# Performance work log

Hardware: AMD Instinct MI355X
Metric: run time of the kernel (lower is better)

Reference implementation:

```python
import jax, jax.numpy as jnp
import numpy as np
from jax import lax

NUM_GROUP = 512
GROUP_SIZE = 32


def setup_inputs() -> dict:
    key = jax.random.key(0)
    x = jax.random.normal(key, (8, 16384, 13), dtype=jnp.float32)
    return {"x": x}


def _fps(pts, num_group):
    """Farthest point sampling. pts: [B,N,3] -> centers [B,G,3], idx [B,G].
    Deterministic start at point 0 (as in pointnet2 CUDA fps)."""
    B, N, _ = pts.shape
    init_idx = jnp.zeros((B,), dtype=jnp.int32)

    def step(carry, _):
        min_d, last = carry                      # [B,N], [B]
        last_pt = jnp.take_along_axis(pts, last[:, None, None], axis=1)  # [B,1,3]
        d = jnp.sum((pts - last_pt) ** 2, axis=-1)                        # [B,N]
        min_d = jnp.minimum(min_d, d)
        nxt = jnp.argmax(min_d, axis=1).astype(jnp.int32)                 # [B]
        return (min_d, nxt), nxt

    init_d = jnp.full((B, N), 1e10, dtype=pts.dtype)
    _, rest = lax.scan(step, (init_d, init_idx), None, length=num_group - 1)  # [G-1,B]
    idx = jnp.concatenate([init_idx[None, :], rest], axis=0).T                # [B,G]
    centers = jnp.take_along_axis(pts, idx[:, :, None], axis=1)               # [B,G,3]
    return centers, idx


def _knn_idx(pts, centers, k):
    """k nearest points (in pts) to each center. pts [B,N,3], centers [B,G,3] -> [B,G,k]."""
    # squared distances [B,G,N] via ||c||^2 + ||p||^2 - 2 c.p
    d2 = (jnp.sum(centers ** 2, -1)[:, :, None]
          + jnp.sum(pts ** 2, -1)[:, None, :]
          - 2.0 * jnp.einsum('bgc,bnc->bgn', centers, pts))
    _, idx = lax.top_k(-d2, k)  # smallest distances
    return idx


def reference(x):
    B, N, C = x.shape
    pts = x[:, :, 4:7]                                  # [B,N,3]
    center_xyz, _ = _fps(pts, NUM_GROUP)                # [B,G,3]
    idx = _knn_idx(pts, center_xyz, GROUP_SIZE)         # [B,G,M]
    # gather neighborhoods: [B,G,M,C]
    flat_idx = idx.reshape(B, NUM_GROUP * GROUP_SIZE)
    neigh = jnp.take_along_axis(x, flat_idx[:, :, None], axis=1)
    neigh = neigh.reshape(B, NUM_GROUP, GROUP_SIZE, C)
    # recenter xyz channels 4:7
    neigh = neigh.at[:, :, :, 4:7].add(-center_xyz[:, :, None, :])
    return neigh, center_xyz
```

## Files before the change

### kernel.cpp

```cpp
#include <hip/hip_runtime.h>
#include <stdint.h>
#include <math.h>

#define BB 8
#define NN 16384
#define CC 13
#define GG 512
#define KK 32

#define NEIGH_ELEMS (BB*GG*KK*CC)

__device__ __forceinline__ void wave_argmax_dpp(float& v, int& p) {
    int vi = __float_as_int(v);
    int pi = p;
#define ARGMAX_STAGE(CTRL)                                                   \
    {                                                                        \
        int nv = __builtin_amdgcn_update_dpp(vi, vi, CTRL, 0xF, 0xF, false); \
        int np = __builtin_amdgcn_update_dpp(pi, pi, CTRL, 0xF, 0xF, false); \
        float a = __int_as_float(nv);                                        \
        float b = __int_as_float(vi);                                        \
        if (a > b || (a == b && np < pi)) { vi = nv; pi = np; }              \
    }
    ARGMAX_STAGE(0x111)
    ARGMAX_STAGE(0x112)
    ARGMAX_STAGE(0x114)
    ARGMAX_STAGE(0x118)
    ARGMAX_STAGE(0x142)
    ARGMAX_STAGE(0x143)
#undef ARGMAX_STAGE
    v = __int_as_float(vi);
    p = pi;
}

__device__ __forceinline__ void wave_argmin_dpp(float& v, int& p) {
    int vi = __float_as_int(v);
    int pi = p;
#define ARGMIN_STAGE(CTRL)                                                   \
    {                                                                        \
        int nv = __builtin_amdgcn_update_dpp(vi, vi, CTRL, 0xF, 0xF, false); \
        int np = __builtin_amdgcn_update_dpp(pi, pi, CTRL, 0xF, 0xF, false); \
        float a = __int_as_float(nv);                                        \
        float b = __int_as_float(vi);                                        \
        if (a < b || (a == b && np < pi)) { vi = nv; pi = np; }              \
    }
    ARGMIN_STAGE(0x111)
    ARGMIN_STAGE(0x112)
    ARGMIN_STAGE(0x114)
    ARGMIN_STAGE(0x118)
    ARGMIN_STAGE(0x142)
    ARGMIN_STAGE(0x143)
#undef ARGMIN_STAGE
    v = __int_as_float(vi);
    p = pi;
}

__global__ void pack_kernel(const float* __restrict__ x,
                            float* __restrict__ px, float* __restrict__ py,
                            float* __restrict__ pz) {
    int i = blockIdx.x * blockDim.x + threadIdx.x;
    if (i >= BB * NN) return;
    const float* p = x + (size_t)i * CC + 4;
    px[i] = p[0]; py[i] = p[1]; pz[i] = p[2];
}

__global__ __launch_bounds__(1024)
__attribute__((amdgpu_waves_per_eu(4, 4)))
void fps_kernel(const float* __restrict__ px,
                const float* __restrict__ py,
                const float* __restrict__ pz,
                float* __restrict__ centers) {
    const int b = blockIdx.x;
    const int t = threadIdx.x;
    const float* PX = px + b * NN;
    const float* PY = py + b * NN;
    const float* PZ = pz + b * NN;

#define DECLPT(i) float x##i, y##i, z##i, md##i;
    DECLPT(0)  DECLPT(1)  DECLPT(2)  DECLPT(3)
    DECLPT(4)  DECLPT(5)  DECLPT(6)  DECLPT(7)
    DECLPT(8)  DECLPT(9)  DECLPT(10) DECLPT(11)
    DECLPT(12) DECLPT(13) DECLPT(14) DECLPT(15)
#undef DECLPT

#define INITPT(i)                                                            \
    {                                                                        \
        int pos = t + (i << 10);                                             \
        x##i = PX[pos]; y##i = PY[pos]; z##i = PZ[pos];                      \
        md##i = 1e10f;                           \
        asm volatile("" : "+v"(x##i), "+v"(y##i), "+v"(z##i));               \
    }
    INITPT(0)  INITPT(1)  INITPT(2)  INITPT(3)
    INITPT(4)  INITPT(5)  INITPT(6)  INITPT(7)
    INITPT(8)  INITPT(9)  INITPT(10) INITPT(11)
    INITPT(12) INITPT(13) INITPT(14) INITPT(15)
#undef INITPT

    __shared__ float s_v[2][16];
    __shared__ int   s_p[2][16];

    int wp = 0;
    if (t == 0) {
        float* oc = centers + (size_t)b * GG * 3;
        oc[0] = PX[0]; oc[1] = PY[0]; oc[2] = PZ[0];
    }

    for (int g = 1; g < GG; ++g) {
        int swp = __builtin_amdgcn_readfirstlane(wp);
        float lx = PX[swp], ly = PY[swp], lz = PZ[swp];
        float bv = -1.0f;
        int bi = 0;
#define STEPPT(i)                                                            \
    {                                                                        \
        float e0 = __fsub_rn(x##i, lx);                                      \
        float e1 = __fsub_rn(y##i, ly);                                      \
        float e2 = __fsub_rn(z##i, lz);                                      \
        float d  = __fadd_rn(__fadd_rn(__fmul_rn(e0, e0), __fmul_rn(e1, e1)),\
                             __fmul_rn(e2, e2));                             \
        float m = fminf(md##i, d);                           \
        md##i = m;                                                           \
        if (m > bv) { bv = m; bi = i; }                                      \
    }
        STEPPT(0)  STEPPT(1)  STEPPT(2)  STEPPT(3)
        STEPPT(4)  STEPPT(5)  STEPPT(6)  STEPPT(7)
        STEPPT(8)  STEPPT(9)  STEPPT(10) STEPPT(11)
        STEPPT(12) STEPPT(13) STEPPT(14) STEPPT(15)
#undef STEPPT
        int bp = t + (bi << 10);
        wave_argmax_dpp(bv, bp);
        int par = g & 1;
        if ((t & 63) == 63) { s_v[par][t >> 6] = bv; s_p[par][t >> 6] = bp; }
        __syncthreads();
        float wv = s_v[par][0]; int wi = s_p[par][0];
#pragma unroll
        for (int q = 1; q < 16; ++q) {
            float qv = s_v[par][q]; int qp = s_p[par][q];
            if (qv > wv || (qv == wv && qp < wi)) { wv = qv; wi = qp; }
        }
        wp = wi;
        if (t == 0) {
            float* oc = centers + ((size_t)b * GG + g) * 3;
            oc[0] = PX[wp]; oc[1] = PY[wp]; oc[2] = PZ[wp];
        }
    }
}

__global__ __launch_bounds__(256, 8) void knn_kernel(const float* __restrict__ px,
                                                     const float* __restrict__ py,
                                                     const float* __restrict__ pz,
                                                     const float* __restrict__ x,
                                                     const float* __restrict__ centers,
                                                     float* __restrict__ out) {
    const int blk = blockIdx.x;
    const int bg  = ((blk & 7) << 9) | (blk >> 3);
    const int b   = bg >> 9;
    const int t   = threadIdx.x;

    const float* ctr = centers + (size_t)bg * 3;
    float cx = ctr[0], cy = ctr[1], cz = ctr[2];
    float cc2 = __fadd_rn(__fadd_rn(__fmul_rn(cx, cx), __fmul_rn(cy, cy)),
                          __fmul_rn(cz, cz));

    const float* PX = px + b * NN;
    const float* PY = py + b * NN;
    const float* PZ = pz + b * NN;

    float k1 = INFINITY, k2 = INFINITY;
    int   p1 = 0x7fffffff, p2 = 0x7fffffff;
    uint64_t mask = 0;

#pragma unroll 4
    for (int i = 0; i < 64; ++i) {
        int pos = (i << 8) + t;
        float ax = PX[pos], ay = PY[pos], az = PZ[pos];
        float pp2 = __fadd_rn(__fadd_rn(__fmul_rn(ax, ax), __fmul_rn(ay, ay)),
                              __fmul_rn(az, az));
        float dot = fmaf(cz, az, fmaf(cy, ay, __fmul_rn(cx, ax)));
        float d2  = __fsub_rn(__fadd_rn(cc2, pp2), __fmul_rn(2.0f, dot));
        if (d2 < k1)      { k2 = k1; p2 = p1; k1 = d2; p1 = pos; }
        else if (d2 < k2) { k2 = d2; p2 = pos; }
    }

    __shared__ float s_v[2][4];
    __shared__ int   s_p[2][4];
    __shared__ int   s_chosen[KK];

    for (int j = 0; j < KK; ++j) {
        float v = k1; int vp = p1;
        wave_argmin_dpp(v, vp);
        int par = j & 1;
        if ((t & 63) == 63) { s_v[par][t >> 6] = v; s_p[par][t >> 6] = vp; }
        __syncthreads();
        float wv = s_v[par][0]; int wp = s_p[par][0];
#pragma unroll
        for (int q = 1; q < 4; ++q) {
            float qv = s_v[par][q]; int qp = s_p[par][q];
            if (qv < wv || (qv == wv && qp < wp)) { wv = qv; wp = qp; }
        }
        if (t == 0) s_chosen[j] = wp;
        if ((wp & 255) == t) {
            mask |= 1ull << (wp >> 8);
            k1 = k2; p1 = p2;
            k2 = INFINITY; p2 = 0x7fffffff;
            if (p1 == 0x7fffffff && mask != 0xffffffffffffffffull) {
                k1 = INFINITY;
#pragma unroll 1
                for (int i = 0; i < 64; ++i) {
                    if ((mask >> i) & 1ull) continue;
                    int pos = (i << 8) + t;
                    float ax = PX[pos], ay = PY[pos], az = PZ[pos];
                    float pp2 = __fadd_rn(__fadd_rn(__fmul_rn(ax, ax), __fmul_rn(ay, ay)),
                                          __fmul_rn(az, az));
                    float dot = fmaf(cz, az, fmaf(cy, ay, __fmul_rn(cx, ax)));
                    float d2  = __fsub_rn(__fadd_rn(cc2, pp2), __fmul_rn(2.0f, dot));
                    if (d2 < k1)      { k2 = k1; p2 = p1; k1 = d2; p1 = pos; }
                    else if (d2 < k2) { k2 = d2; p2 = pos; }
                }
            }
        }
    }
    __syncthreads();

    for (int v = t; v < KK * CC; v += 256) {
        int j = v / CC, c = v - j * CC;
        int pt = s_chosen[j] & (NN - 1);
        float val = x[((size_t)b * NN + pt) * CC + c];
        if (c >= 4 && c < 7) {
            float cs = (c == 4) ? cx : ((c == 5) ? cy : cz);
            val = __fsub_rn(val, cs);
        }
        out[((size_t)bg * KK + j) * CC + c] = val;
    }
}

extern "C" void kernel_launch(void* const* d_in, const int* in_sizes, int n_in,
                              void* d_out, int out_size, void* d_ws, size_t ws_size,
                              hipStream_t stream) {
    const float* x = (const float*)d_in[0];
    float* out = (float*)d_out;
    float* centers = out + NEIGH_ELEMS;

    float* px = (float*)d_ws;
    float* py = px + BB * NN;
    float* pz = py + BB * NN;

    pack_kernel<<<(BB * NN + 255) / 256, 256, 0, stream>>>(x, px, py, pz);
    fps_kernel<<<BB, 1024, 0, stream>>>(px, py, pz, centers);
    knn_kernel<<<BB * GG, 256, 0, stream>>>(px, py, pz, x, centers, out);
}
```

Measured before the change: 1.658 ms.

## Split farthest point sampling across two blocks per batch with global mailbox exchange

The FPS kernel now launches two 1024-thread blocks per batch, each holding half of the points (8 per thread instead of 16). After each iteration's block-local argmax, the two blocks swap their candidate through a packed 64-bit word in global memory, using relaxed agent-scope atomics and a spin-wait. The aim is to halve the per-iteration distance update and register pressure by spreading the serial loop over more CUs. In exchange, every iteration now pays a cross-CU L2 round trip and relies on both blocks being resident at once; the mailbox lives at the start of the output buffer, which knn later overwrites.

```diff
diff --git a/kernel.cpp b/kernel.cpp
--- a/kernel.cpp
+++ b/kernel.cpp
@@ -54,52 +54,63 @@
     p = pi;
 }
 
+__device__ __forceinline__ unsigned long long mbox_load(const unsigned long long* p) {
+    return __hip_atomic_load(p, __ATOMIC_RELAXED, __HIP_MEMORY_SCOPE_AGENT);
+}
+__device__ __forceinline__ void mbox_store(unsigned long long* p, unsigned long long v) {
+    __hip_atomic_store(p, v, __ATOMIC_RELAXED, __HIP_MEMORY_SCOPE_AGENT);
+}
+
 __global__ void pack_kernel(const float* __restrict__ x,
                             float* __restrict__ px, float* __restrict__ py,
-                            float* __restrict__ pz) {
+                            float* __restrict__ pz,
+                            unsigned long long* __restrict__ mbox) {
     int i = blockIdx.x * blockDim.x + threadIdx.x;
+    if (blockIdx.x == 0 && threadIdx.x < 32) mbox[threadIdx.x * 8] = 0ull;
     if (i >= BB * NN) return;
     const float* p = x + (size_t)i * CC + 4;
     px[i] = p[0]; py[i] = p[1]; pz[i] = p[2];
 }
 
 __global__ __launch_bounds__(1024)
-__attribute__((amdgpu_waves_per_eu(4, 4)))
 void fps_kernel(const float* __restrict__ px,
                 const float* __restrict__ py,
                 const float* __restrict__ pz,
-                float* __restrict__ centers) {
-    const int b = blockIdx.x;
+                float* __restrict__ centers,
+                unsigned long long* __restrict__ mbox) {
+    const int blk = blockIdx.x;
+    const int b = blk & 7;
+    const int k = blk >> 3;
     const int t = threadIdx.x;
+    const int base = k << 13;
     const float* PX = px + b * NN;
     const float* PY = py + b * NN;
     const float* PZ = pz + b * NN;
 
+    unsigned long long* my_base  = mbox + (((b << 2) | (k << 1)) << 3);
+    unsigned long long* oth_base = mbox + (((b << 2) | ((k ^ 1) << 1)) << 3);
+
 #define DECLPT(i) float x##i, y##i, z##i, md##i;
-    DECLPT(0)  DECLPT(1)  DECLPT(2)  DECLPT(3)
-    DECLPT(4)  DECLPT(5)  DECLPT(6)  DECLPT(7)
-    DECLPT(8)  DECLPT(9)  DECLPT(10) DECLPT(11)
-    DECLPT(12) DECLPT(13) DECLPT(14) DECLPT(15)
+    DECLPT(0) DECLPT(1) DECLPT(2) DECLPT(3)
+    DECLPT(4) DECLPT(5) DECLPT(6) DECLPT(7)
 #undef DECLPT
 
 #define INITPT(i)                                                            \
     {                                                                        \
-        int pos = t + (i << 10);                                             \
+        int pos = base + t + (i << 10);                                      \
         x##i = PX[pos]; y##i = PY[pos]; z##i = PZ[pos];                      \
         md##i = 1e10f;                           \
         asm volatile("" : "+v"(x##i), "+v"(y##i), "+v"(z##i));               \
     }
-    INITPT(0)  INITPT(1)  INITPT(2)  INITPT(3)
-    INITPT(4)  INITPT(5)  INITPT(6)  INITPT(7)
-    INITPT(8)  INITPT(9)  INITPT(10) INITPT(11)
-    INITPT(12) INITPT(13) INITPT(14) INITPT(15)
+    INITPT(0) INITPT(1) INITPT(2) INITPT(3)
+    INITPT(4) INITPT(5) INITPT(6) INITPT(7)
 #undef INITPT
 
     __shared__ float s_v[2][16];
     __shared__ int   s_p[2][16];
 
     int wp = 0;
-    if (t == 0) {
+    if (k == 0 && t == 0) {
         float* oc = centers + (size_t)b * GG * 3;
         oc[0] = PX[0]; oc[1] = PY[0]; oc[2] = PZ[0];
     }
@@ -120,24 +131,35 @@
         md##i = m;                                                           \
         if (m > bv) { bv = m; bi = i; }                                      \
     }
-        STEPPT(0)  STEPPT(1)  STEPPT(2)  STEPPT(3)
-        STEPPT(4)  STEPPT(5)  STEPPT(6)  STEPPT(7)
-        STEPPT(8)  STEPPT(9)  STEPPT(10) STEPPT(11)
-        STEPPT(12) STEPPT(13) STEPPT(14) STEPPT(15)
+        STEPPT(0) STEPPT(1) STEPPT(2) STEPPT(3)
+        STEPPT(4) STEPPT(5) STEPPT(6) STEPPT(7)
 #undef STEPPT
-        int bp = t + (bi << 10);
+        int bp = base + t + (bi << 10);
         wave_argmax_dpp(bv, bp);
         int par = g & 1;
         if ((t & 63) == 63) { s_v[par][t >> 6] = bv; s_p[par][t >> 6] = bp; }
         __syncthreads();
-        float wv = s_v[par][0]; int wi = s_p[par][0];
+        float lv = s_v[par][0]; int lp = s_p[par][0];
 #pragma unroll
         for (int q = 1; q < 16; ++q) {
             float qv = s_v[par][q]; int qp = s_p[par][q];
-            if (qv > wv || (qv == wv && qp < wi)) { wv = qv; wi = qp; }
-        }
-        wp = wi;
+            if (qv > lv || (qv == lv && qp < lp)) { lv = qv; lp = qp; }
+        }
         if (t == 0) {
+            unsigned long long pk = ((unsigned long long)g << 46)
+                                  | ((unsigned long long)(unsigned)__float_as_int(lv) << 14)
+                                  | (unsigned long long)(unsigned)lp;
+            mbox_store(my_base + par * 8, pk);
+        }
+        unsigned long long v;
+        int guard = 0;
+        do {
+            v = mbox_load(oth_base + par * 8);
+        } while ((int)(v >> 46) != g && ++guard < (1 << 26));
+        float pvf = __int_as_float((int)((v >> 14) & 0xFFFFFFFFull));
+        int   pp  = (int)(v & 0x3FFFull);
+        wp = (pvf > lv || (pvf == lv && pp < lp)) ? pp : lp;
+        if (k == 0 && t == 0) {
             float* oc = centers + ((size_t)b * GG + g) * 3;
             oc[0] = PX[wp]; oc[1] = PY[wp]; oc[2] = PZ[wp];
         }
@@ -243,7 +265,9 @@
     float* py = px + BB * NN;
     float* pz = py + BB * NN;
 
-    pack_kernel<<<(BB * NN + 255) / 256, 256, 0, stream>>>(x, px, py, pz);
-    fps_kernel<<<BB, 1024, 0, stream>>>(px, py, pz, centers);
+    unsigned long long* mbox = (unsigned long long*)d_out;
+
+    pack_kernel<<<(BB * NN + 255) / 256, 256, 0, stream>>>(x, px, py, pz, mbox);
+    fps_kernel<<<2 * BB, 1024, 0, stream>>>(px, py, pz, centers, mbox);
     knn_kernel<<<BB * GG, 256, 0, stream>>>(px, py, pz, x, centers, out);
 }
```

Result: slower. 1.734 ms (+4.6%).
